# Kernel optimization log

Measured on AMD Instinct MI355X. Metric: run time of the kernel, lower is better.

Reference implementation:

```python
import jax, jax.numpy as jnp
import numpy as np

# Problem sizes (see shape_source): 32 point clouds of 2048 points each.
B, P, K = 32, 2048, 20
DIN, H, OUT = 3, 128, 128
N = B * P
EPS = 1e-5  # BatchNorm eps (eval mode: running stats mean=0, var=1)


def setup_inputs() -> dict:
    key = jax.random.key(0)
    ks = jax.random.split(key, 8)
    x = jax.random.normal(ks[0], (N, DIN), dtype=jnp.float32)
    batch = (jnp.arange(N) // P).astype(jnp.int32)  # equal-size clouds

    def lin(k, i, o):
        return (jax.random.normal(k, (i, o), dtype=jnp.float32) / np.sqrt(i)).astype(jnp.float32)

    return {
        "x": x, "batch": batch,
        # transfer = MLP([input_dim, hid_dim]) -> single Linear
        "Wt": lin(ks[1], DIN, H), "bt": jnp.zeros((H,), jnp.float32),
        # GINConv layer 0: Linear(H,2H) -> ReLU -> Linear(2H,H)
        "W1_0": lin(ks[2], H, 2 * H), "b1_0": jnp.zeros((2 * H,), jnp.float32),
        "W2_0": lin(ks[3], 2 * H, H), "b2_0": jnp.zeros((H,), jnp.float32),
        "g0": jnp.ones((H,), jnp.float32), "be0": jnp.zeros((H,), jnp.float32),
        "rm0": jnp.zeros((H,), jnp.float32), "rv0": jnp.ones((H,), jnp.float32),
        # GINConv layer 1
        "W1_1": lin(ks[4], H, 2 * H), "b1_1": jnp.zeros((2 * H,), jnp.float32),
        "W2_1": lin(ks[5], 2 * H, OUT), "b2_1": jnp.zeros((OUT,), jnp.float32),
        "g1": jnp.ones((OUT,), jnp.float32), "be1": jnp.zeros((OUT,), jnp.float32),
        "rm1": jnp.zeros((OUT,), jnp.float32), "rv1": jnp.ones((OUT,), jnp.float32),
    }


def _knn_idx(x):
    """Per-cloud kNN (includes self, dist 0), returns global neighbor ids [N,K]."""
    xb = x.reshape(B, P, DIN)
    sq = jnp.sum(xb * xb, axis=-1)  # [B,P]
    # squared euclidean distance [B,P,P]
    dist = sq[:, :, None] + sq[:, None, :] - 2.0 * jnp.einsum('bpd,bqd->bpq', xb, xb)
    _, idx = jax.lax.top_k(-dist, K)  # [B,P,K] nearest (incl. self)
    offs = (jnp.arange(B, dtype=idx.dtype) * P)[:, None, None]
    return (idx + offs).reshape(N, K)


def _bn_eval(h, g, be, rm, rv):
    return g * (h - rm) * jax.lax.rsqrt(rv + EPS) + be


def _gin_max(h, nbr, W1, b1, W2, b2):
    # max-aggregation over kNN neighbors + self loop, then GIN MLP
    agg = jnp.maximum(jnp.max(h[nbr], axis=1), h)  # [N,d]
    return jax.nn.relu(agg @ W1 + b1) @ W2 + b2


def reference(x, batch, Wt, bt,
              W1_0, b1_0, W2_0, b2_0, g0, be0, rm0, rv0,
              W1_1, b1_1, W2_1, b2_1, g1, be1, rm1, rv1):
    nbr = _knn_idx(jax.lax.stop_gradient(x))  # knn(x, x, k, batch).flip([0])
    h = x @ Wt + bt  # transfer MLP (single Linear)
    # layer 0: GINConv(max) -> BN -> ReLU (dropout identity in eval)
    h = _gin_max(h, nbr, W1_0, b1_0, W2_0, b2_0)
    h = jax.nn.relu(_bn_eval(h, g0, be0, rm0, rv0))
    # layer 1 (last): GINConv(max) -> BN -> dropout (identity)
    h = _gin_max(h, nbr, W1_1, b1_1, W2_1, b2_1)
    h = _bn_eval(h, g1, be1, rm1, rv1)
    return h
```

## Files before the change

kernel.cpp:

```cpp
#include <hip/hip_runtime.h>

typedef unsigned int u32;
typedef unsigned short u16;
typedef unsigned long long u64;

#define NPTS 65536
#define PCLD 2048
#define KNN 20
#define HD 128
#define HD2 256

typedef __attribute__((ext_vector_type(8))) short bf16x8;
typedef __attribute__((ext_vector_type(4))) float f32x4;
typedef unsigned short us2 __attribute__((ext_vector_type(2)));

__device__ __forceinline__ u16 f2bf(float f) {
    u32 u = __float_as_uint(f);
    u32 r = (u + 0x7FFFu + ((u >> 16) & 1u)) >> 16;
    return (u16)r;
}
__device__ __forceinline__ u32 enc2(u32 b) {
    u32 s = (b >> 15) & 0x00010001u;
    return b ^ (s * 0x7FFFu) ^ 0x80008000u;
}
__device__ __forceinline__ u32 dec2(u32 e) {
    u32 s = ((~e) >> 15) & 0x00010001u;
    return e ^ (s * 0x7FFFu) ^ 0x80008000u;
}
__device__ __forceinline__ u32 max2(u32 a, u32 b) {
#if __has_builtin(__builtin_elementwise_max)
    us2 x, y; __builtin_memcpy(&x, &a, 4); __builtin_memcpy(&y, &b, 4);
    us2 r = __builtin_elementwise_max(x, y);
    u32 o; __builtin_memcpy(&o, &r, 4); return o;
#else
    u32 lo = ((a & 0xFFFFu) > (b & 0xFFFFu)) ? (a & 0xFFFFu) : (b & 0xFFFFu);
    u32 hi = ((a >> 16) > (b >> 16)) ? (a & 0xFFFF0000u) : (b & 0xFFFF0000u);
    return lo | hi;
#endif
}

__global__ __launch_bounds__(256) void prep_kernel(
    const float* __restrict__ W1_0, const float* __restrict__ W2_0,
    const float* __restrict__ W1_1, const float* __restrict__ W2_1,
    u16* __restrict__ W1_0T, u16* __restrict__ W2_0T,
    u16* __restrict__ W1_1T, u16* __restrict__ W2_1T) {
    int id = blockIdx.x * 256 + threadIdx.x;
    int m = id >> 15, e = id & 32767;
    if (m == 0)      { int n = e >> 7, k = e & 127; W1_0T[e] = f2bf(W1_0[k * 256 + n]); }
    else if (m == 1) { int n = e >> 8, k = e & 255; W2_0T[e] = f2bf(W2_0[k * 128 + n]); }
    else if (m == 2) { int n = e >> 7, k = e & 127; W1_1T[e] = f2bf(W1_1[k * 256 + n]); }
    else             { int n = e >> 8, k = e & 255; W2_1T[e] = f2bf(W2_1[k * 128 + n]); }
}

__global__ __launch_bounds__(256) void knn_kernel(const float* __restrict__ x,
                                                  u16* __restrict__ nbr) {
    __shared__ float4 pts[PCLD];
    const int cloud = blockIdx.x >> 3;
    const int qi = ((blockIdx.x & 7) << 8) + threadIdx.x;
    const float* xc = x + (u64)cloud * PCLD * 3;
    for (int t = threadIdx.x; t < PCLD; t += 256) {
        float a = xc[3 * t], b = xc[3 * t + 1], c = xc[3 * t + 2];
        float sq = __fadd_rn(__fadd_rn(__fmul_rn(a, a), __fmul_rn(b, b)), __fmul_rn(c, c));
        pts[t] = make_float4(a, b, c, sq);
    }
    __syncthreads();
    const float4 q = pts[qi];
    const float qx = q.x, qy = q.y, qz = q.z, qs = q.w;
    const int lane = threadIdx.x & 63;
    u64 list[KNN];
#pragma unroll
    for (int k = 0; k < KNN; ++k) list[k] = 0xFF800000FFFFFFFFull;
    float thr = __builtin_inff();

    for (int base = 0; base < PCLD; base += 64) {
        float4 cp = pts[base + lane];
        u64 mask = 0;
#pragma unroll
        for (int c = 0; c < 64; ++c) {
            float cx = __uint_as_float(__builtin_amdgcn_readlane(__float_as_uint(cp.x), c));
            float cy = __uint_as_float(__builtin_amdgcn_readlane(__float_as_uint(cp.y), c));
            float cz = __uint_as_float(__builtin_amdgcn_readlane(__float_as_uint(cp.z), c));
            float cs = __uint_as_float(__builtin_amdgcn_readlane(__float_as_uint(cp.w), c));
            float dot = __builtin_fmaf(cz, qz, __builtin_fmaf(cy, qy, __fmul_rn(cx, qx)));
            float d = __fsub_rn(__fadd_rn(qs, cs), __fmul_rn(2.0f, dot));
            if (d < thr) mask |= (1ull << c);
        }
        while (mask) {
            int c = __builtin_ctzll(mask);
            mask &= mask - 1;
            float4 p2 = pts[base + c];
            float dot = __builtin_fmaf(p2.z, qz, __builtin_fmaf(p2.y, qy, __fmul_rn(p2.x, qx)));
            float d = __fsub_rn(__fadd_rn(qs, p2.w), __fmul_rn(2.0f, dot));
            if (d < thr) {
                u32 ub = __float_as_uint(d);
                u32 e = (ub & 0x80000000u) ? ~ub : (ub | 0x80000000u);
                u64 key = (((u64)e) << 32) | (u32)(base + c);
#pragma unroll
                for (int k = 0; k < KNN; ++k) {
                    u64 lo = key < list[k] ? key : list[k];
                    u64 hi = key < list[k] ? list[k] : key;
                    list[k] = lo; key = hi;
                }
                u32 e19 = (u32)(list[KNN - 1] >> 32);
                u32 ud = (e19 & 0x80000000u) ? (e19 & 0x7FFFFFFFu) : ~e19;
                thr = __uint_as_float(ud);
            }
        }
    }
    u16* out = nbr + (u64)(cloud * PCLD + qi) * KNN;
#pragma unroll
    for (int k = 0; k < KNN; ++k) out[k] = (u16)(u32)list[k];
}

__global__ __launch_bounds__(256) void feat_kernel(const float* __restrict__ x,
                                                   const float* __restrict__ Wt,
                                                   const float* __restrict__ bt,
                                                   u16* __restrict__ h0e) {
    int gid = blockIdx.x * 256 + threadIdx.x;
    int i = gid >> 4;
    int g = gid & 15;
    int c0 = g << 3;
    float x0 = x[3 * i], x1 = x[3 * i + 1], x2 = x[3 * i + 2];
    u32 o[4];
#pragma unroll
    for (int j = 0; j < 8; j += 2) {
        int c = c0 + j;
        float a0 = bt[c]     + x0 * Wt[c]     + x1 * Wt[128 + c]     + x2 * Wt[256 + c];
        float a1 = bt[c + 1] + x0 * Wt[c + 1] + x1 * Wt[128 + c + 1] + x2 * Wt[256 + c + 1];
        o[j >> 1] = enc2(((u32)f2bf(a0)) | (((u32)f2bf(a1)) << 16));
    }
    uint4* dst = (uint4*)&h0e[(u64)i * HD + c0];
    *dst = make_uint4(o[0], o[1], o[2], o[3]);
}

template <int RELU_OUT, int OUT_F32>
__global__ __launch_bounds__(256) void gemm_kernel(
    const u16* __restrict__ he, const u16* __restrict__ nbr_,
    const u16* __restrict__ W1T, const float* __restrict__ b1,
    const u16* __restrict__ W2T, const float* __restrict__ b2,
    const float* __restrict__ g, const float* __restrict__ be,
    const float* __restrict__ rm, const float* __restrict__ rv,
    void* __restrict__ hout_v) {
    __shared__ u16 aggL[64][136];
    __shared__ u16 hidL[64][264];
    const int tid = threadIdx.x;
    const int b = blockIdx.x;
    const int xcd = b & 7, j = b >> 3;
    const int cloud = xcd + 8 * (j >> 5);
    const int tile = j & 31;
    const int R = cloud * PCLD + tile * 64;

    {
        const int r = tid >> 2, cg = tid & 3;
        const int co = cg * 8;
        const int grow = R + r;
        const u16* __restrict__ hrow = he + (u64)grow * HD;
        uint4 m0 = *(const uint4*)&hrow[co];
        uint4 m1 = *(const uint4*)&hrow[32 + co];
        uint4 m2 = *(const uint4*)&hrow[64 + co];
        uint4 m3 = *(const uint4*)&hrow[96 + co];
        const u64* nb8 = (const u64*)(nbr_ + (u64)grow * KNN);
        u64 nq[5];
#pragma unroll
        for (int w = 0; w < 5; ++w) nq[w] = nb8[w];
        const u16* __restrict__ hcl = he + (u64)cloud * PCLD * HD;
#pragma unroll 4
        for (int t = 0; t < KNN; ++t) {
            int loc = (int)(nq[t >> 2] >> ((t & 3) * 16)) & (PCLD - 1);
            const u16* __restrict__ vrow = hcl + (u64)loc * HD;
            uint4 v0 = *(const uint4*)&vrow[co];
            uint4 v1 = *(const uint4*)&vrow[32 + co];
            uint4 v2 = *(const uint4*)&vrow[64 + co];
            uint4 v3 = *(const uint4*)&vrow[96 + co];
            m0.x = max2(m0.x, v0.x); m0.y = max2(m0.y, v0.y);
            m0.z = max2(m0.z, v0.z); m0.w = max2(m0.w, v0.w);
            m1.x = max2(m1.x, v1.x); m1.y = max2(m1.y, v1.y);
            m1.z = max2(m1.z, v1.z); m1.w = max2(m1.w, v1.w);
            m2.x = max2(m2.x, v2.x); m2.y = max2(m2.y, v2.y);
            m2.z = max2(m2.z, v2.z); m2.w = max2(m2.w, v2.w);
            m3.x = max2(m3.x, v3.x); m3.y = max2(m3.y, v3.y);
            m3.z = max2(m3.z, v3.z); m3.w = max2(m3.w, v3.w);
        }
        *(uint4*)&aggL[r][co]      = make_uint4(dec2(m0.x), dec2(m0.y), dec2(m0.z), dec2(m0.w));
        *(uint4*)&aggL[r][32 + co] = make_uint4(dec2(m1.x), dec2(m1.y), dec2(m1.z), dec2(m1.w));
        *(uint4*)&aggL[r][64 + co] = make_uint4(dec2(m2.x), dec2(m2.y), dec2(m2.z), dec2(m2.w));
        *(uint4*)&aggL[r][96 + co] = make_uint4(dec2(m3.x), dec2(m3.y), dec2(m3.z), dec2(m3.w));
    }
    __syncthreads();

    const int wv = tid >> 6, lane = tid & 63;
    const int lr = lane & 15;
    const int lq = lane >> 4;

    {
        f32x4 acc[4][4];
#pragma unroll
        for (int i = 0; i < 4; ++i)
#pragma unroll
            for (int j2 = 0; j2 < 4; ++j2) acc[i][j2] = (f32x4)(0.0f);
        const int nb0 = wv * 64;
#pragma unroll
        for (int ks = 0; ks < 4; ++ks) {
            const int kcol = ks * 32 + lq * 8;
            bf16x8 af[4], bfr[4];
#pragma unroll
            for (int mt = 0; mt < 4; ++mt)
                af[mt] = *(const bf16x8*)&aggL[mt * 16 + lr][kcol];
#pragma unroll
            for (int nt = 0; nt < 4; ++nt)
                bfr[nt] = *(const bf16x8*)&W1T[(u64)(nb0 + nt * 16 + lr) * HD + kcol];
#pragma unroll
            for (int mt = 0; mt < 4; ++mt)
#pragma unroll
                for (int nt = 0; nt < 4; ++nt)
                    acc[mt][nt] = __builtin_amdgcn_mfma_f32_16x16x32_bf16(af[mt], bfr[nt], acc[mt][nt], 0, 0, 0);
        }
#pragma unroll
        for (int nt = 0; nt < 4; ++nt) {
            const int c = nb0 + nt * 16 + lr;
            const float bias = b1[c];
#pragma unroll
            for (int mt = 0; mt < 4; ++mt)
#pragma unroll
                for (int r2 = 0; r2 < 4; ++r2) {
                    float v = fmaxf(acc[mt][nt][r2] + bias, 0.0f);
                    hidL[mt * 16 + lq * 4 + r2][c] = f2bf(v);
                }
        }
    }
    __syncthreads();

    {
        f32x4 acc[4][2];
#pragma unroll
        for (int i = 0; i < 4; ++i) { acc[i][0] = (f32x4)(0.0f); acc[i][1] = (f32x4)(0.0f); }
        const int nb0 = wv * 32;
#pragma unroll
        for (int ks = 0; ks < 8; ++ks) {
            const int kcol = ks * 32 + lq * 8;
            bf16x8 af[4], bfr[2];
#pragma unroll
            for (int mt = 0; mt < 4; ++mt)
                af[mt] = *(const bf16x8*)&hidL[mt * 16 + lr][kcol];
#pragma unroll
            for (int nt = 0; nt < 2; ++nt)
                bfr[nt] = *(const bf16x8*)&W2T[(u64)(nb0 + nt * 16 + lr) * HD2 + kcol];
#pragma unroll
            for (int mt = 0; mt < 4; ++mt)
#pragma unroll
                for (int nt = 0; nt < 2; ++nt)
                    acc[mt][nt] = __builtin_amdgcn_mfma_f32_16x16x32_bf16(af[mt], bfr[nt], acc[mt][nt], 0, 0, 0);
        }
#pragma unroll
        for (int nt = 0; nt < 2; ++nt) {
            const int c = nb0 + nt * 16 + lr;
            const float bias = b2[c];
            const float sc = g[c] * (1.0f / sqrtf(rv[c] + 1e-5f));
            const float rmc = rm[c];
            const float bec = be[c];
#pragma unroll
            for (int mt = 0; mt < 4; ++mt)
#pragma unroll
                for (int r2 = 0; r2 < 4; ++r2) {
                    float v = acc[mt][nt][r2] + bias;
                    v = (v - rmc) * sc + bec;
                    if (RELU_OUT) v = fmaxf(v, 0.0f);
                    const int row = R + mt * 16 + lq * 4 + r2;
                    if (OUT_F32) {
                        ((float*)hout_v)[(u64)row * HD + c] = v;
                    } else {
                        u16 bb = f2bf(v);
                        u16 e = bb ^ ((bb & 0x8000u) ? (u16)0xFFFFu : (u16)0x8000u);
                        ((u16*)hout_v)[(u64)row * HD + c] = e;
                    }
                }
        }
    }
}

extern "C" void kernel_launch(void* const* d_in, const int* in_sizes, int n_in,
                              void* d_out, int out_size, void* d_ws, size_t ws_size,
                              hipStream_t stream) {
    const float* x    = (const float*)d_in[0];
    const float* Wt   = (const float*)d_in[2];
    const float* bt   = (const float*)d_in[3];
    const float* W1_0 = (const float*)d_in[4];
    const float* b1_0 = (const float*)d_in[5];
    const float* W2_0 = (const float*)d_in[6];
    const float* b2_0 = (const float*)d_in[7];
    const float* g0   = (const float*)d_in[8];
    const float* be0  = (const float*)d_in[9];
    const float* rm0  = (const float*)d_in[10];
    const float* rv0  = (const float*)d_in[11];
    const float* W1_1 = (const float*)d_in[12];
    const float* b1_1 = (const float*)d_in[13];
    const float* W2_1 = (const float*)d_in[14];
    const float* b2_1 = (const float*)d_in[15];
    const float* g1   = (const float*)d_in[16];
    const float* be1  = (const float*)d_in[17];
    const float* rm1  = (const float*)d_in[18];
    const float* rv1  = (const float*)d_in[19];

    char* ws = (char*)d_ws;
    u16* he0  = (u16*)ws;
    u16* he1  = (u16*)(ws + 16777216);
    u16* W10T = (u16*)(ws + 2 * 16777216);
    u16* W20T = W10T + 32768;
    u16* W11T = W20T + 32768;
    u16* W21T = W11T + 32768;
    u16* nbr  = (u16*)(ws + 2 * 16777216 + 4 * 65536);

    knn_kernel<<<256, 256, 0, stream>>>(x, nbr);
    prep_kernel<<<512, 256, 0, stream>>>(W1_0, W2_0, W1_1, W2_1, W10T, W20T, W11T, W21T);
    feat_kernel<<<4096, 256, 0, stream>>>(x, Wt, bt, he0);
    gemm_kernel<1, 0><<<1024, 256, 0, stream>>>(he0, nbr, W10T, b1_0, W20T, b2_0,
                                                g0, be0, rm0, rv0, he1);
    gemm_kernel<0, 1><<<1024, 256, 0, stream>>>(he1, nbr, W11T, b1_1, W21T, b2_1,
                                                g1, be1, rm1, rv1, d_out);
}
```

Baseline: 324.0 us.

## Reorder points by Morton code so neighbor gathers are spatially local

Adds a per-cloud sort kernel that quantizes coordinates, builds Morton keys and bitonic-sorts them to get a permutation. Features and neighbor lists are stored in sorted order, so each 64-row GEMM tile gathers neighbors that lie close in memory, improving cache reuse. The final output is scattered back to the original order through the permutation. This costs an extra launch with many barriers, plus the indirection and a scattered final store.

```diff
diff --git a/kernel.cpp b/kernel.cpp
--- a/kernel.cpp
+++ b/kernel.cpp
@@ -37,6 +37,78 @@
     u32 hi = ((a >> 16) > (b >> 16)) ? (a & 0xFFFF0000u) : (b & 0xFFFF0000u);
     return lo | hi;
 #endif
+}
+
+__device__ __forceinline__ u32 spread3(u32 v) {
+    v &= 0x3FF;
+    v = (v | (v << 16)) & 0x030000FF;
+    v = (v | (v << 8))  & 0x0300F00F;
+    v = (v | (v << 4))  & 0x030C30C3;
+    v = (v | (v << 2))  & 0x09249249;
+    return v;
+}
+
+__global__ __launch_bounds__(256) void sort_kernel(const float* __restrict__ x,
+                                                   u16* __restrict__ perm,
+                                                   u16* __restrict__ iperm) {
+    __shared__ u32 keys[PCLD];
+    __shared__ float red[256];
+    const int cloud = blockIdx.x;
+    const int tid = threadIdx.x;
+    const float* xc = x + (u64)cloud * PCLD * 3;
+
+    float mn[3] = {1e30f, 1e30f, 1e30f}, mx[3] = {-1e30f, -1e30f, -1e30f};
+    for (int m = 0; m < 8; ++m) {
+        int t = tid + 256 * m;
+        float a = xc[3 * t], b = xc[3 * t + 1], c = xc[3 * t + 2];
+        mn[0] = fminf(mn[0], a); mx[0] = fmaxf(mx[0], a);
+        mn[1] = fminf(mn[1], b); mx[1] = fmaxf(mx[1], b);
+        mn[2] = fminf(mn[2], c); mx[2] = fmaxf(mx[2], c);
+    }
+    float bmn[3], sc[3];
+    for (int d = 0; d < 3; ++d) {
+        red[tid] = mn[d]; __syncthreads();
+        for (int s = 128; s > 0; s >>= 1) { if (tid < s) red[tid] = fminf(red[tid], red[tid + s]); __syncthreads(); }
+        bmn[d] = red[0]; __syncthreads();
+        red[tid] = mx[d]; __syncthreads();
+        for (int s = 128; s > 0; s >>= 1) { if (tid < s) red[tid] = fmaxf(red[tid], red[tid + s]); __syncthreads(); }
+        float rng = red[0] - bmn[d];
+        sc[d] = 127.0f / fmaxf(rng, 1e-6f);
+        __syncthreads();
+    }
+
+    for (int m = 0; m < 8; ++m) {
+        int t = tid + 256 * m;
+        float a = xc[3 * t], b = xc[3 * t + 1], c = xc[3 * t + 2];
+        u32 qa = (u32)fminf(fmaxf((a - bmn[0]) * sc[0], 0.0f), 127.0f);
+        u32 qb = (u32)fminf(fmaxf((b - bmn[1]) * sc[1], 0.0f), 127.0f);
+        u32 qc = (u32)fminf(fmaxf((c - bmn[2]) * sc[2], 0.0f), 127.0f);
+        u32 mort = spread3(qa) | (spread3(qb) << 1) | (spread3(qc) << 2);
+        keys[t] = (mort << 11) | (u32)t;
+    }
+    __syncthreads();
+
+    for (int k = 2; k <= PCLD; k <<= 1) {
+        for (int j = k >> 1; j > 0; j >>= 1) {
+            for (int m = 0; m < 4; ++m) {
+                int i = tid + 256 * m;
+                int idx = ((i & ~(j - 1)) << 1) | (i & (j - 1));
+                int l = idx | j;
+                bool asc = ((idx & k) == 0);
+                u32 a = keys[idx], b = keys[l];
+                bool sw = asc ? (a > b) : (a < b);
+                if (sw) { keys[idx] = b; keys[l] = a; }
+            }
+            __syncthreads();
+        }
+    }
+
+    for (int m = 0; m < 8; ++m) {
+        int s = tid + 256 * m;
+        u16 o = (u16)(keys[s] & 0x7FF);
+        perm[cloud * PCLD + s] = o;
+        iperm[cloud * PCLD + o] = (u16)s;
+    }
 }
 
 __global__ __launch_bounds__(256) void prep_kernel(
@@ -53,8 +125,10 @@
 }
 
 __global__ __launch_bounds__(256) void knn_kernel(const float* __restrict__ x,
+                                                  const u16* __restrict__ iperm,
                                                   u16* __restrict__ nbr) {
     __shared__ float4 pts[PCLD];
+    __shared__ u16 ipermL[PCLD];
     const int cloud = blockIdx.x >> 3;
     const int qi = ((blockIdx.x & 7) << 8) + threadIdx.x;
     const float* xc = x + (u64)cloud * PCLD * 3;
@@ -62,6 +136,7 @@
         float a = xc[3 * t], b = xc[3 * t + 1], c = xc[3 * t + 2];
         float sq = __fadd_rn(__fadd_rn(__fmul_rn(a, a), __fmul_rn(b, b)), __fmul_rn(c, c));
         pts[t] = make_float4(a, b, c, sq);
+        ipermL[t] = iperm[cloud * PCLD + t];
     }
     __syncthreads();
     const float4 q = pts[qi];
@@ -107,14 +182,15 @@
             }
         }
     }
-    u16* out = nbr + (u64)(cloud * PCLD + qi) * KNN;
-#pragma unroll
-    for (int k = 0; k < KNN; ++k) out[k] = (u16)(u32)list[k];
+    u16* out = nbr + ((u64)cloud * PCLD + ipermL[qi]) * KNN;
+#pragma unroll
+    for (int k = 0; k < KNN; ++k) out[k] = ipermL[(u32)list[k] & (PCLD - 1)];
 }
 
 __global__ __launch_bounds__(256) void feat_kernel(const float* __restrict__ x,
                                                    const float* __restrict__ Wt,
                                                    const float* __restrict__ bt,
+                                                   const u16* __restrict__ iperm,
                                                    u16* __restrict__ h0e) {
     int gid = blockIdx.x * 256 + threadIdx.x;
     int i = gid >> 4;
@@ -129,13 +205,16 @@
         float a1 = bt[c + 1] + x0 * Wt[c + 1] + x1 * Wt[128 + c + 1] + x2 * Wt[256 + c + 1];
         o[j >> 1] = enc2(((u32)f2bf(a0)) | (((u32)f2bf(a1)) << 16));
     }
-    uint4* dst = (uint4*)&h0e[(u64)i * HD + c0];
+    const int cl = i >> 11;
+    const int ri = cl * PCLD + (int)iperm[i];
+    uint4* dst = (uint4*)&h0e[(u64)ri * HD + c0];
     *dst = make_uint4(o[0], o[1], o[2], o[3]);
 }
 
 template <int RELU_OUT, int OUT_F32>
 __global__ __launch_bounds__(256) void gemm_kernel(
     const u16* __restrict__ he, const u16* __restrict__ nbr_,
+    const u16* __restrict__ perm_,
     const u16* __restrict__ W1T, const float* __restrict__ b1,
     const u16* __restrict__ W2T, const float* __restrict__ b2,
     const float* __restrict__ g, const float* __restrict__ be,
@@ -265,13 +344,14 @@
                     float v = acc[mt][nt][r2] + bias;
                     v = (v - rmc) * sc + bec;
                     if (RELU_OUT) v = fmaxf(v, 0.0f);
-                    const int row = R + mt * 16 + lq * 4 + r2;
+                    const int lrow = tile * 64 + mt * 16 + lq * 4 + r2;
                     if (OUT_F32) {
-                        ((float*)hout_v)[(u64)row * HD + c] = v;
+                        const int orow = cloud * PCLD + (int)perm_[cloud * PCLD + lrow];
+                        ((float*)hout_v)[(u64)orow * HD + c] = v;
                     } else {
                         u16 bb = f2bf(v);
                         u16 e = bb ^ ((bb & 0x8000u) ? (u16)0xFFFFu : (u16)0x8000u);
-                        ((u16*)hout_v)[(u64)row * HD + c] = e;
+                        ((u16*)hout_v)[(u64)(cloud * PCLD + lrow) * HD + c] = e;
                     }
                 }
         }
@@ -309,12 +389,15 @@
     u16* W11T = W20T + 32768;
     u16* W21T = W11T + 32768;
     u16* nbr  = (u16*)(ws + 2 * 16777216 + 4 * 65536);
-
-    knn_kernel<<<256, 256, 0, stream>>>(x, nbr);
+    u16* perm = nbr + (u64)NPTS * KNN;
+    u16* iperm = perm + NPTS;
+
+    sort_kernel<<<32, 256, 0, stream>>>(x, perm, iperm);
+    knn_kernel<<<256, 256, 0, stream>>>(x, iperm, nbr);
     prep_kernel<<<512, 256, 0, stream>>>(W1_0, W2_0, W1_1, W2_1, W10T, W20T, W11T, W21T);
-    feat_kernel<<<4096, 256, 0, stream>>>(x, Wt, bt, he0);
-    gemm_kernel<1, 0><<<1024, 256, 0, stream>>>(he0, nbr, W10T, b1_0, W20T, b2_0,
+    feat_kernel<<<4096, 256, 0, stream>>>(x, Wt, bt, iperm, he0);
+    gemm_kernel<1, 0><<<1024, 256, 0, stream>>>(he0, nbr, perm, W10T, b1_0, W20T, b2_0,
                                                 g0, be0, rm0, rv0, he1);
-    gemm_kernel<0, 1><<<1024, 256, 0, stream>>>(he1, nbr, W11T, b1_1, W21T, b2_1,
+    gemm_kernel<0, 1><<<1024, 256, 0, stream>>>(he1, nbr, perm, W11T, b1_1, W21T, b2_1,
                                                 g1, be1, rm1, rv1, d_out);
 }
```

Result: slower. 387.3 us (+19.5%).
